# Optimization experiments

Measured on AMD Instinct MI355X. Metric: run time of the kernel, lower is better.

Reference implementation:

```python
import jax
import jax.numpy as jnp
import numpy as np

EPS = 1e-06


def _topk_mask(scores, k):
    # scores: (T, E); hard top-k mask along last dim
    _, idx = jax.lax.top_k(scores, k)            # (T, k)
    hard = jax.nn.one_hot(idx, scores.shape[-1]).sum(axis=-2)  # (T, E)
    return hard.astype(bool)


def setup_inputs() -> dict:
    key = jax.random.key(0)
    k1, k2, k3 = jax.random.split(key, 3)
    T, D, E = 8192, 4096, 64
    h_td = jax.random.normal(k1, (T, D), dtype=jnp.float32)
    # eqx.nn.Linear weight layout: (out_features, in_features)
    W = jax.random.normal(k2, (E, D), dtype=jnp.float32) * (1.0 / np.sqrt(D))
    bias_e = jax.random.normal(k3, (E,), dtype=jnp.float32)
    return {"h_td": h_td, "W": W, "bias_e": bias_e, "k": 8}


def reference(h_td, W, bias_e, k):
    # Linear(d_model -> E), no bias in proj; external bias_e added after
    logits_te = jnp.einsum("td,ed->te", h_td, W) + bias_e[None, :]  # (T, E)
    # Soft combine weights always from clean logits
    weight_te = jax.nn.softmax(logits_te, axis=-1)
    # Training path: Gumbel noise on the selection scores only
    gkey = jax.random.key(42)
    u = jax.random.uniform(gkey, logits_te.shape, minval=EPS, maxval=1.0 - EPS)
    g = -jnp.log(-jnp.log(u))
    sel_scores = logits_te + g
    mask_te = _topk_mask(sel_scores, k)
    return (mask_te, weight_te, logits_te)
```

## Files before the change

### kernel.cpp

```cpp
#include <hip/hip_runtime.h>
#include <stdint.h>
#include <math.h>

#define T_DIM 8192
#define D_DIM 4096
#define E_DIM 64
#define TE (T_DIM * E_DIM)
#define GAP_MARGIN 4e-3
#define BK 128
#define NCHUNK (D_DIM / BK)
#define KSTEPS (BK / 32)
#define ROWS 16

typedef __attribute__((ext_vector_type(8))) short short8_t;
typedef __attribute__((ext_vector_type(4))) float f32x4;

__device__ __align__(16) short Whi_g[E_DIM * D_DIM];
__device__ __align__(16) short Wlo_g[E_DIM * D_DIM];

__device__ __forceinline__ void threefry2x32_k42(uint32_t x0, uint32_t x1,
                                                 uint32_t& o0, uint32_t& o1) {
  const uint32_t ks0 = 0u, ks1 = 42u;
  const uint32_t ks2 = 0x1BD11BDAu ^ ks0 ^ ks1;
  x0 += ks0; x1 += ks1;
#define TF_RND(r) { x0 += x1; x1 = (x1 << (r)) | (x1 >> (32 - (r))); x1 ^= x0; }
  TF_RND(13) TF_RND(15) TF_RND(26) TF_RND(6)   x0 += ks1; x1 += ks2 + 1u;
  TF_RND(17) TF_RND(29) TF_RND(16) TF_RND(24)  x0 += ks2; x1 += ks0 + 2u;
  TF_RND(13) TF_RND(15) TF_RND(26) TF_RND(6)   x0 += ks0; x1 += ks1 + 3u;
  TF_RND(17) TF_RND(29) TF_RND(16) TF_RND(24)  x0 += ks1; x1 += ks2 + 4u;
  TF_RND(13) TF_RND(15) TF_RND(26) TF_RND(6)   x0 += ks2; x1 += ks0 + 5u;
#undef TF_RND
  o0 = x0; o1 = x1;
}

__device__ __forceinline__ uint32_t jax_random_bits32(uint32_t j) {
  uint32_t o0, o1;
  threefry2x32_k42(0u, j, o0, o1);
  return o0 ^ o1;
}

__device__ __forceinline__ void finalize_row_f64(double logit, int e, int t,
                                                 float& mask_out, float& weight_out,
                                                 double& gap_out) {
  double m = logit;
#pragma unroll
  for (int off = 1; off < 64; off <<= 1) {
    const double om = __shfl_xor(m, off, 64);
    m = (om > m) ? om : m;
  }
  const double pe = exp(logit - m);
  double s = pe;
#pragma unroll
  for (int off = 1; off < 64; off <<= 1) s += __shfl_xor(s, off, 64);
  weight_out = (float)(pe / s);

  const int idx = t * 64 + e;
  const uint32_t bits = jax_random_bits32((uint32_t)idx);
  const float f01 = __uint_as_float((bits >> 9) | 0x3f800000u) - 1.0f;
  const float minv = 1e-6f;
  const float maxv = 0.999999f;
  float u = __fadd_rn(__fmul_rn(f01, maxv - minv), minv);
  u = fmaxf(minv, u);
  const double g = -log(-log((double)u));
  const double sel = logit + g;

  float mask = 0.0f;
  double cur = sel;
  double v8 = 0.0, v9 = 0.0;
  for (int it = 0; it < 9; ++it) {
    double v = cur;
    int vi = e;
#pragma unroll
    for (int off = 1; off < 64; off <<= 1) {
      const double ov = __shfl_xor(v, off, 64);
      const int    oi = __shfl_xor(vi, off, 64);
      if (ov > v || (ov == v && oi < vi)) { v = ov; vi = oi; }
    }
    if (it < 8) {
      if (vi == e) { mask = 1.0f; cur = -__builtin_inf(); }
      if (it == 7) v8 = v;
    } else {
      v9 = v;
    }
  }
  mask_out = mask;
  gap_out = v8 - v9;
}

__device__ __forceinline__ uint16_t f2bf(float f) {
  const uint32_t x = __float_as_uint(f);
  return (uint16_t)((x + 0x7FFFu + ((x >> 16) & 1u)) >> 16);
}

__device__ __forceinline__ void split8(const float4 a, const float4 b,
                                       short8_t& hi, short8_t& lo) {
  const float f[8] = {a.x, a.y, a.z, a.w, b.x, b.y, b.z, b.w};
#pragma unroll
  for (int j = 0; j < 8; ++j) {
    const uint16_t hb = f2bf(f[j]);
    const float fh = __uint_as_float((uint32_t)hb << 16);
    const uint16_t lb = f2bf(f[j] - fh);
    hi[j] = (short)hb;
    lo[j] = (short)lb;
  }
}

__global__ __launch_bounds__(256)
void w_split_kernel(const float* __restrict__ W) {
  const int g = blockIdx.x * 256 + threadIdx.x;
#pragma unroll
  for (int r = 0; r < 2; ++r) {
    const int u = g * 2 + r;
    const int e = u >> 9;
    const int k0 = (u & 511) * 8;
    const float* wp = W + (size_t)e * D_DIM + k0;
    const float4 a = *reinterpret_cast<const float4*>(wp);
    const float4 b = *reinterpret_cast<const float4*>(wp + 4);
    short8_t hi, lo;
    split8(a, b, hi, lo);
    const int ch = k0 >> 7, s = (k0 >> 5) & 3, q = (k0 >> 3) & 3;
    const int subE = e >> 4, ee = e & 15;
    const int idx = ch * 8192 + s * 2048 + subE * 512 + q * 128 + ee * 8;
    *reinterpret_cast<short8_t*>(Whi_g + idx) = hi;
    *reinterpret_cast<short8_t*>(Wlo_g + idx) = lo;
  }
}

__global__ __launch_bounds__(256, 2)
void router_mfma_kernel(const float* __restrict__ h,
                        const float* __restrict__ bias,
                        float* __restrict__ out,
                        unsigned char* __restrict__ flags) {
  __shared__ __align__(16) short Ahi[2][KSTEPS * 512];
  __shared__ __align__(16) short Alo[2][KSTEPS * 512];
  __shared__ float logits_lds[ROWS * 65];

  const int tid  = threadIdx.x;
  const int wave = tid >> 6;
  const int lane = tid & 63;
  const int row0 = blockIdx.x * ROWS;

  const int a_row  = tid >> 4;
  const int a_koct = tid & 15;
  const int a_s = a_koct >> 2, a_q = a_koct & 3;
  const int u_w0 = a_s * 64 + a_q * 16 + a_row;
  const int u_w  = u_w0 ^ ((u_w0 >> 4) & 7);
  const int a_widx = u_w * 8;
  const float* hrow = h + (size_t)(row0 + a_row) * D_DIM + a_koct * 8;

  const int b_off = wave * 512 + (lane >> 4) * 128 + (lane & 15) * 8;

  f32x4 acc = {0.0f, 0.0f, 0.0f, 0.0f};

  float4 pa0 = *reinterpret_cast<const float4*>(hrow);
  float4 pa1 = *reinterpret_cast<const float4*>(hrow + 4);

  int buf = 0;
  for (int ch = 0; ch < NCHUNK; ++ch) {
    short8_t hi, lo;
    split8(pa0, pa1, hi, lo);
    *reinterpret_cast<short8_t*>(&Ahi[buf][a_widx]) = hi;
    *reinterpret_cast<short8_t*>(&Alo[buf][a_widx]) = lo;
    __syncthreads();

    if (ch + 1 < NCHUNK) {
      const float* p = hrow + (size_t)(ch + 1) * BK;
      pa0 = *reinterpret_cast<const float4*>(p);
      pa1 = *reinterpret_cast<const float4*>(p + 4);
    }

    const short* bhp = Whi_g + (size_t)ch * 8192 + b_off;
    const short* blp = Wlo_g + (size_t)ch * 8192 + b_off;
#pragma unroll
    for (int s = 0; s < KSTEPS; ++s) {
      const int ur0 = s * 64 + lane;
      const int ur  = ur0 ^ ((ur0 >> 4) & 7);
      const short8_t ah = *reinterpret_cast<const short8_t*>(&Ahi[buf][ur * 8]);
      const short8_t al = *reinterpret_cast<const short8_t*>(&Alo[buf][ur * 8]);
      const short8_t bh = *reinterpret_cast<const short8_t*>(bhp + s * 2048);
      const short8_t bl = *reinterpret_cast<const short8_t*>(blp + s * 2048);
      acc = __builtin_amdgcn_mfma_f32_16x16x32_bf16(al, bh, acc, 0, 0, 0);
      acc = __builtin_amdgcn_mfma_f32_16x16x32_bf16(ah, bl, acc, 0, 0, 0);
      acc = __builtin_amdgcn_mfma_f32_16x16x32_bf16(ah, bh, acc, 0, 0, 0);
    }
    buf ^= 1;
  }

  {
    const int q   = lane >> 4;
    const int col = wave * 16 + (lane & 15);
#pragma unroll
    for (int reg = 0; reg < 4; ++reg) {
      const int m = q * 4 + reg;
      logits_lds[m * 65 + col] = acc[reg];
    }
  }
  __syncthreads();

  const int e = lane;
  const double be = (double)bias[e];
  for (int rr = 0; rr < 4; ++rr) {
    const int rloc = wave * 4 + rr;
    const int t = row0 + rloc;
    const double logit = (double)logits_lds[rloc * 65 + e] + be;

    float mask, weight;
    double gap;
    finalize_row_f64(logit, e, t, mask, weight, gap);

    const int idx = t * 64 + e;
    out[idx]          = mask;
    out[TE + idx]     = weight;
    out[2 * TE + idx] = (float)logit;
    if (e == 0) flags[t] = (gap < GAP_MARGIN) ? 1 : 0;
  }
}

__global__ __launch_bounds__(256)
void router_fixup_kernel(const float* __restrict__ h,
                         const float* __restrict__ W,
                         const float* __restrict__ bias,
                         const unsigned char* __restrict__ flags,
                         float* __restrict__ out) {
  const int t = blockIdx.x;
  if (flags[t] == 0) return;

  __shared__ double red[4][64];

  const int tid  = threadIdx.x;
  const int wv   = tid >> 6;
  const int lane = tid & 63;

  const float* hrow = h + (size_t)t * D_DIM + wv * 1024;

  float hv[16];
#pragma unroll
  for (int j = 0; j < 16; ++j) hv[j] = hrow[j * 64 + lane];

  for (int e0 = 0; e0 < 64; e0 += 4) {
    const float* w0 = W + (size_t)(e0 + 0) * D_DIM + wv * 1024;
    const float* w1 = W + (size_t)(e0 + 1) * D_DIM + wv * 1024;
    const float* w2 = W + (size_t)(e0 + 2) * D_DIM + wv * 1024;
    const float* w3 = W + (size_t)(e0 + 3) * D_DIM + wv * 1024;
    double a0 = 0.0, a1 = 0.0, a2 = 0.0, a3 = 0.0;
#pragma unroll
    for (int j = 0; j < 16; ++j) {
      const double hd = (double)hv[j];
      a0 = fma((double)w0[j * 64 + lane], hd, a0);
      a1 = fma((double)w1[j * 64 + lane], hd, a1);
      a2 = fma((double)w2[j * 64 + lane], hd, a2);
      a3 = fma((double)w3[j * 64 + lane], hd, a3);
    }
#pragma unroll
    for (int off = 1; off < 64; off <<= 1) {
      a0 += __shfl_xor(a0, off, 64);
      a1 += __shfl_xor(a1, off, 64);
      a2 += __shfl_xor(a2, off, 64);
      a3 += __shfl_xor(a3, off, 64);
    }
    if (lane == e0 + 0) red[wv][lane] = a0;
    if (lane == e0 + 1) red[wv][lane] = a1;
    if (lane == e0 + 2) red[wv][lane] = a2;
    if (lane == e0 + 3) red[wv][lane] = a3;
  }
  __syncthreads();

  if (wv == 0) {
    const int e = lane;
    const double logit = ((red[0][e] + red[1][e]) + (red[2][e] + red[3][e]))
                         + (double)bias[e];
    float mask, weight;
    double gap;
    finalize_row_f64(logit, e, t, mask, weight, gap);

    const int idx = t * 64 + e;
    out[idx]          = mask;
    out[TE + idx]     = weight;
    out[2 * TE + idx] = (float)logit;
  }
}

extern "C" void kernel_launch(void* const* d_in, const int* in_sizes, int n_in,
                              void* d_out, int out_size, void* d_ws, size_t ws_size,
                              hipStream_t stream) {
  const float* h    = (const float*)d_in[0];
  const float* W    = (const float*)d_in[1];
  const float* bias = (const float*)d_in[2];
  float* out = (float*)d_out;
  unsigned char* flags = (unsigned char*)d_ws;

  w_split_kernel<<<64, 256, 0, stream>>>(W);
  router_mfma_kernel<<<T_DIM / ROWS, 256, 0, stream>>>(h, bias, out, flags);
  router_fixup_kernel<<<T_DIM, 256, 0, stream>>>(h, W, bias, flags, out);
}
```

Before: 293.8 us.

## Load A fragments directly from global, drop LDS staging, grid-stride fixup kernel

The main MFMA kernel no longer stages the h tile through double-buffered LDS with barriers. Each wave now loads its own A fragments straight from global memory and splits them to bf16 hi/lo in registers. Because all four waves read the same 16 rows, h is loaded redundantly, leaning on cache hits in exchange for removing LDS traffic and syncs. The W split layout is flattened to per-k-step indexing, the occupancy hint in launch bounds is dropped, and the fixup kernel becomes a 256-block grid-stride loop so fewer blocks are launched that would exit immediately.

New measurement: 814.1 us. 177% more time.

```diff
diff --git a/kernel.cpp b/kernel.cpp
--- a/kernel.cpp
+++ b/kernel.cpp
@@ -7,10 +7,8 @@
 #define E_DIM 64
 #define TE (T_DIM * E_DIM)
 #define GAP_MARGIN 4e-3
-#define BK 128
-#define NCHUNK (D_DIM / BK)
-#define KSTEPS (BK / 32)
 #define ROWS 16
+#define NKSTEP (D_DIM / 32)
 
 typedef __attribute__((ext_vector_type(8))) short short8_t;
 typedef __attribute__((ext_vector_type(4))) float f32x4;
@@ -118,21 +116,19 @@
     const float4 b = *reinterpret_cast<const float4*>(wp + 4);
     short8_t hi, lo;
     split8(a, b, hi, lo);
-    const int ch = k0 >> 7, s = (k0 >> 5) & 3, q = (k0 >> 3) & 3;
+    const int ks = k0 >> 5, q = (k0 >> 3) & 3;
     const int subE = e >> 4, ee = e & 15;
-    const int idx = ch * 8192 + s * 2048 + subE * 512 + q * 128 + ee * 8;
+    const int idx = ks * 2048 + subE * 512 + q * 128 + ee * 8;
     *reinterpret_cast<short8_t*>(Whi_g + idx) = hi;
     *reinterpret_cast<short8_t*>(Wlo_g + idx) = lo;
   }
 }
 
-__global__ __launch_bounds__(256, 2)
+__global__ __launch_bounds__(256)
 void router_mfma_kernel(const float* __restrict__ h,
                         const float* __restrict__ bias,
                         float* __restrict__ out,
                         unsigned char* __restrict__ flags) {
-  __shared__ __align__(16) short Ahi[2][KSTEPS * 512];
-  __shared__ __align__(16) short Alo[2][KSTEPS * 512];
   __shared__ float logits_lds[ROWS * 65];
 
   const int tid  = threadIdx.x;
@@ -140,50 +136,27 @@
   const int lane = tid & 63;
   const int row0 = blockIdx.x * ROWS;
 
-  const int a_row  = tid >> 4;
-  const int a_koct = tid & 15;
-  const int a_s = a_koct >> 2, a_q = a_koct & 3;
-  const int u_w0 = a_s * 64 + a_q * 16 + a_row;
-  const int u_w  = u_w0 ^ ((u_w0 >> 4) & 7);
-  const int a_widx = u_w * 8;
-  const float* hrow = h + (size_t)(row0 + a_row) * D_DIM + a_koct * 8;
+  const int a_row  = lane & 15;
+  const int a_koct = lane >> 4;
+  const float* aptr = h + (size_t)(row0 + a_row) * D_DIM + a_koct * 8;
 
   const int b_off = wave * 512 + (lane >> 4) * 128 + (lane & 15) * 8;
+  const short* bh_base = Whi_g + b_off;
+  const short* bl_base = Wlo_g + b_off;
 
   f32x4 acc = {0.0f, 0.0f, 0.0f, 0.0f};
 
-  float4 pa0 = *reinterpret_cast<const float4*>(hrow);
-  float4 pa1 = *reinterpret_cast<const float4*>(hrow + 4);
-
-  int buf = 0;
-  for (int ch = 0; ch < NCHUNK; ++ch) {
-    short8_t hi, lo;
-    split8(pa0, pa1, hi, lo);
-    *reinterpret_cast<short8_t*>(&Ahi[buf][a_widx]) = hi;
-    *reinterpret_cast<short8_t*>(&Alo[buf][a_widx]) = lo;
-    __syncthreads();
-
-    if (ch + 1 < NCHUNK) {
-      const float* p = hrow + (size_t)(ch + 1) * BK;
-      pa0 = *reinterpret_cast<const float4*>(p);
-      pa1 = *reinterpret_cast<const float4*>(p + 4);
-    }
-
-    const short* bhp = Whi_g + (size_t)ch * 8192 + b_off;
-    const short* blp = Wlo_g + (size_t)ch * 8192 + b_off;
-#pragma unroll
-    for (int s = 0; s < KSTEPS; ++s) {
-      const int ur0 = s * 64 + lane;
-      const int ur  = ur0 ^ ((ur0 >> 4) & 7);
-      const short8_t ah = *reinterpret_cast<const short8_t*>(&Ahi[buf][ur * 8]);
-      const short8_t al = *reinterpret_cast<const short8_t*>(&Alo[buf][ur * 8]);
-      const short8_t bh = *reinterpret_cast<const short8_t*>(bhp + s * 2048);
-      const short8_t bl = *reinterpret_cast<const short8_t*>(blp + s * 2048);
-      acc = __builtin_amdgcn_mfma_f32_16x16x32_bf16(al, bh, acc, 0, 0, 0);
-      acc = __builtin_amdgcn_mfma_f32_16x16x32_bf16(ah, bl, acc, 0, 0, 0);
-      acc = __builtin_amdgcn_mfma_f32_16x16x32_bf16(ah, bh, acc, 0, 0, 0);
-    }
-    buf ^= 1;
+#pragma unroll 4
+  for (int ks = 0; ks < NKSTEP; ++ks) {
+    const float4 a0 = *reinterpret_cast<const float4*>(aptr + ks * 32);
+    const float4 a1 = *reinterpret_cast<const float4*>(aptr + ks * 32 + 4);
+    const short8_t bh = *reinterpret_cast<const short8_t*>(bh_base + (size_t)ks * 2048);
+    const short8_t bl = *reinterpret_cast<const short8_t*>(bl_base + (size_t)ks * 2048);
+    short8_t ah, al;
+    split8(a0, a1, ah, al);
+    acc = __builtin_amdgcn_mfma_f32_16x16x32_bf16(al, bh, acc, 0, 0, 0);
+    acc = __builtin_amdgcn_mfma_f32_16x16x32_bf16(ah, bl, acc, 0, 0, 0);
+    acc = __builtin_amdgcn_mfma_f32_16x16x32_bf16(ah, bh, acc, 0, 0, 0);
   }
 
   {
@@ -222,61 +195,63 @@
                          const float* __restrict__ bias,
                          const unsigned char* __restrict__ flags,
                          float* __restrict__ out) {
-  const int t = blockIdx.x;
-  if (flags[t] == 0) return;
-
   __shared__ double red[4][64];
 
   const int tid  = threadIdx.x;
   const int wv   = tid >> 6;
   const int lane = tid & 63;
 
-  const float* hrow = h + (size_t)t * D_DIM + wv * 1024;
-
-  float hv[16];
-#pragma unroll
-  for (int j = 0; j < 16; ++j) hv[j] = hrow[j * 64 + lane];
-
-  for (int e0 = 0; e0 < 64; e0 += 4) {
-    const float* w0 = W + (size_t)(e0 + 0) * D_DIM + wv * 1024;
-    const float* w1 = W + (size_t)(e0 + 1) * D_DIM + wv * 1024;
-    const float* w2 = W + (size_t)(e0 + 2) * D_DIM + wv * 1024;
-    const float* w3 = W + (size_t)(e0 + 3) * D_DIM + wv * 1024;
-    double a0 = 0.0, a1 = 0.0, a2 = 0.0, a3 = 0.0;
-#pragma unroll
-    for (int j = 0; j < 16; ++j) {
-      const double hd = (double)hv[j];
-      a0 = fma((double)w0[j * 64 + lane], hd, a0);
-      a1 = fma((double)w1[j * 64 + lane], hd, a1);
-      a2 = fma((double)w2[j * 64 + lane], hd, a2);
-      a3 = fma((double)w3[j * 64 + lane], hd, a3);
-    }
-#pragma unroll
-    for (int off = 1; off < 64; off <<= 1) {
-      a0 += __shfl_xor(a0, off, 64);
-      a1 += __shfl_xor(a1, off, 64);
-      a2 += __shfl_xor(a2, off, 64);
-      a3 += __shfl_xor(a3, off, 64);
-    }
-    if (lane == e0 + 0) red[wv][lane] = a0;
-    if (lane == e0 + 1) red[wv][lane] = a1;
-    if (lane == e0 + 2) red[wv][lane] = a2;
-    if (lane == e0 + 3) red[wv][lane] = a3;
-  }
-  __syncthreads();
-
-  if (wv == 0) {
-    const int e = lane;
-    const double logit = ((red[0][e] + red[1][e]) + (red[2][e] + red[3][e]))
-                         + (double)bias[e];
-    float mask, weight;
-    double gap;
-    finalize_row_f64(logit, e, t, mask, weight, gap);
-
-    const int idx = t * 64 + e;
-    out[idx]          = mask;
-    out[TE + idx]     = weight;
-    out[2 * TE + idx] = (float)logit;
+  for (int t = blockIdx.x; t < T_DIM; t += 256) {
+    if (flags[t] == 0) continue;
+
+    const float* hrow = h + (size_t)t * D_DIM + wv * 1024;
+
+    float hv[16];
+#pragma unroll
+    for (int j = 0; j < 16; ++j) hv[j] = hrow[j * 64 + lane];
+
+    for (int e0 = 0; e0 < 64; e0 += 4) {
+      const float* w0 = W + (size_t)(e0 + 0) * D_DIM + wv * 1024;
+      const float* w1 = W + (size_t)(e0 + 1) * D_DIM + wv * 1024;
+      const float* w2 = W + (size_t)(e0 + 2) * D_DIM + wv * 1024;
+      const float* w3 = W + (size_t)(e0 + 3) * D_DIM + wv * 1024;
+      double a0 = 0.0, a1 = 0.0, a2 = 0.0, a3 = 0.0;
+#pragma unroll
+      for (int j = 0; j < 16; ++j) {
+        const double hd = (double)hv[j];
+        a0 = fma((double)w0[j * 64 + lane], hd, a0);
+        a1 = fma((double)w1[j * 64 + lane], hd, a1);
+        a2 = fma((double)w2[j * 64 + lane], hd, a2);
+        a3 = fma((double)w3[j * 64 + lane], hd, a3);
+      }
+#pragma unroll
+      for (int off = 1; off < 64; off <<= 1) {
+        a0 += __shfl_xor(a0, off, 64);
+        a1 += __shfl_xor(a1, off, 64);
+        a2 += __shfl_xor(a2, off, 64);
+        a3 += __shfl_xor(a3, off, 64);
+      }
+      if (lane == e0 + 0) red[wv][lane] = a0;
+      if (lane == e0 + 1) red[wv][lane] = a1;
+      if (lane == e0 + 2) red[wv][lane] = a2;
+      if (lane == e0 + 3) red[wv][lane] = a3;
+    }
+    __syncthreads();
+
+    if (wv == 0) {
+      const int e = lane;
+      const double logit = ((red[0][e] + red[1][e]) + (red[2][e] + red[3][e]))
+                           + (double)bias[e];
+      float mask, weight;
+      double gap;
+      finalize_row_f64(logit, e, t, mask, weight, gap);
+
+      const int idx = t * 64 + e;
+      out[idx]          = mask;
+      out[TE + idx]     = weight;
+      out[2 * TE + idx] = (float)logit;
+    }
+    __syncthreads();
   }
 }
 
@@ -291,5 +266,5 @@
 
   w_split_kernel<<<64, 256, 0, stream>>>(W);
   router_mfma_kernel<<<T_DIM / ROWS, 256, 0, stream>>>(h, bias, out, flags);
-  router_fixup_kernel<<<T_DIM, 256, 0, stream>>>(h, W, bias, flags, out);
-}
+  router_fixup_kernel<<<256, 256, 0, stream>>>(h, W, bias, flags, out);
+}
```
